# Optimization experiments

Hardware: AMD Instinct MI355X
Metric: run time of the kernel (lower is better)

## Reference

```python
import jax, jax.numpy as jnp
import numpy as np

EMB = 768
N_HEADS = 12
HEAD_DIM = EMB // N_HEADS


def setup_inputs() -> dict:
    key = jax.random.key(0)
    k_x, k_w1, k_b1, k_w2, k_b2 = jax.random.split(key, 5)
    B, T = 8, 1024
    s = 0.02
    return {
        "x": jax.random.normal(k_x, (B, T, EMB), dtype=jnp.float32),
        "w_attn": jax.random.normal(k_w1, (EMB, 3 * EMB), dtype=jnp.float32) * s,
        "b_attn": jax.random.normal(k_b1, (3 * EMB,), dtype=jnp.float32) * s,
        "w_proj": jax.random.normal(k_w2, (EMB, EMB), dtype=jnp.float32) * s,
        "b_proj": jax.random.normal(k_b2, (EMB,), dtype=jnp.float32) * s,
    }


def reference(x, w_attn, b_attn, w_proj, b_proj):
    B, T, C = x.shape
    qkv = x @ w_attn + b_attn                       # [B,T,3C]
    q, k, v = jnp.split(qkv, 3, axis=2)
    # [B,T,C] -> [B,H,T,D]
    q = q.reshape(B, T, N_HEADS, HEAD_DIM).transpose(0, 2, 1, 3)
    k = k.reshape(B, T, N_HEADS, HEAD_DIM).transpose(0, 2, 1, 3)
    v = v.reshape(B, T, N_HEADS, HEAD_DIM).transpose(0, 2, 1, 3)
    scale = HEAD_DIM ** -0.5
    att = jnp.einsum("bhqd,bhkd->bhqk", q, k) * scale  # [B,H,T,T]
    causal = jnp.tril(jnp.ones((T, T), dtype=bool))
    att = jnp.where(causal, att, -jnp.inf)
    att = jax.nn.softmax(att, axis=-1)
    out = jnp.einsum("bhqk,bhkd->bhqd", att, v)        # [B,H,T,D]
    out = out.transpose(0, 2, 1, 3).reshape(B, T, C)
    return out @ w_proj + b_proj
```

## Files before the change

### kernel.cpp

```cpp
#include <hip/hip_runtime.h>
#include <hip/hip_bf16.h>
#include <math.h>

#define BATCH 8
#define SEQ   1024
#define EMB   768
#define NH    12
#define HD    64
#define QKVW  (3 * EMB)
#define VOFF  (2 * EMB)

typedef short short8   __attribute__((ext_vector_type(8)));
typedef float floatx4  __attribute__((ext_vector_type(4)));

__device__ __forceinline__ short f2bf(float f) {
    union { float f; unsigned u; } v; v.f = f;
    unsigned r = (v.u + 0x7fffu + ((v.u >> 16) & 1u)) >> 16;
    return (short)r;
}

__device__ __forceinline__ void async_load16(const void* g, void* l) {
    __builtin_amdgcn_global_load_lds(
        (const __attribute__((address_space(1))) unsigned int*)g,
        (__attribute__((address_space(3))) unsigned int*)l, 16, 0, 0);
}

__global__ __launch_bounds__(256) void cvt_bf16(
    const float* __restrict__ in, short* __restrict__ out, int n8)
{
    const int i = blockIdx.x * 256 + threadIdx.x;
    if (i >= n8) return;
    const float4 a = ((const float4*)in)[2 * i];
    const float4 b = ((const float4*)in)[2 * i + 1];
    short8 s;
    s[0] = f2bf(a.x); s[1] = f2bf(a.y); s[2] = f2bf(a.z); s[3] = f2bf(a.w);
    s[4] = f2bf(b.x); s[5] = f2bf(b.y); s[6] = f2bf(b.z); s[7] = f2bf(b.w);
    ((short8*)out)[i] = s;
}

__global__ __launch_bounds__(256) void transpose_to_bf16(
    const float* __restrict__ in, short* __restrict__ outT, int R, int C)
{
    __shared__ float t[32][33];
    const int c0 = blockIdx.x * 32, r0 = blockIdx.y * 32;
    const int lx = threadIdx.x & 31, ly = threadIdx.x >> 5;
    #pragma unroll
    for (int i = 0; i < 32; i += 8)
        t[ly + i][lx] = in[(size_t)(r0 + ly + i) * C + c0 + lx];
    __syncthreads();
    #pragma unroll
    for (int i = 0; i < 32; i += 8)
        outT[(size_t)(c0 + ly + i) * R + r0 + lx] = f2bf(t[lx][ly + i]);
}

#define GBK 64

template <int MODE>
__global__ __launch_bounds__(256) void gemm_bf16(
    const short* __restrict__ A, const short* __restrict__ Bt,
    const float* __restrict__ bias, void* __restrict__ Cout,
    short* __restrict__ vt, int M, int N, int K)
{
    __shared__ __align__(16) short As[128 * GBK];
    __shared__ __align__(16) short Bs[128 * GBK];

    const int tid  = threadIdx.x;
    const int wave = tid >> 6;
    const int lane = tid & 63;
    const int ln15 = lane & 15;
    const int quad = lane >> 4;
    const int wr   = (wave >> 1) * 64;
    const int wc   = (wave & 1) * 64;
    const int row0 = blockIdx.y * 128;
    const int col0 = blockIdx.x * 128;

    const bool trans = (MODE == 0) || (col0 < VOFF);

    floatx4 acc[4][4];
    #pragma unroll
    for (int i = 0; i < 4; ++i)
        #pragma unroll
        for (int j = 0; j < 4; ++j) acc[i][j] = (floatx4){0.f, 0.f, 0.f, 0.f};

    for (int k0 = 0; k0 < K; k0 += GBK) {
        __syncthreads();
        #pragma unroll
        for (int p = 0; p < 4; ++p) {
            const int id  = p * 256 + tid;
            const int row = id >> 3;
            const int c   = (id & 7) ^ (row & 7);
            async_load16(A  + (size_t)(row0 + row) * K + k0 + c * 8, &As[id * 8]);
            async_load16(Bt + (size_t)(col0 + row) * K + k0 + c * 8, &Bs[id * 8]);
        }
        __syncthreads();

        #pragma unroll
        for (int half = 0; half < 2; ++half) {
            short8 af[4], bf[4];
            #pragma unroll
            for (int t = 0; t < 4; ++t) {
                const int ch = ((quad + half * 4) ^ (ln15 & 7)) * 8;
                af[t] = *(const short8*)&As[(wr + t * 16 + ln15) * GBK + ch];
                bf[t] = *(const short8*)&Bs[(wc + t * 16 + ln15) * GBK + ch];
            }
            if (trans) {
                #pragma unroll
                for (int i = 0; i < 4; ++i)
                    #pragma unroll
                    for (int j = 0; j < 4; ++j)
                        acc[i][j] = __builtin_amdgcn_mfma_f32_16x16x32_bf16(bf[j], af[i], acc[i][j], 0, 0, 0);
            } else {
                #pragma unroll
                for (int i = 0; i < 4; ++i)
                    #pragma unroll
                    for (int j = 0; j < 4; ++j)
                        acc[i][j] = __builtin_amdgcn_mfma_f32_16x16x32_bf16(af[i], bf[j], acc[i][j], 0, 0, 0);
            }
        }
    }

    if (MODE == 1 && !trans) {
        #pragma unroll
        for (int j = 0; j < 4; ++j) {
            const int c  = col0 + wc + j * 16 + ln15;
            const float bv = bias[c];
            const int c2 = c - VOFF;
            #pragma unroll
            for (int i = 0; i < 4; ++i) {
                const int r = row0 + wr + i * 16 + quad * 4;
                union { short s[4]; unsigned long long u; } pk;
                #pragma unroll
                for (int reg = 0; reg < 4; ++reg)
                    pk.s[reg] = f2bf(acc[i][j][reg] + bv);
                *(unsigned long long*)&vt[(size_t)(r >> 10) * (EMB * SEQ) +
                                          (size_t)c2 * SEQ + (r & 1023)] = pk.u;
            }
        }
    } else {
        float4 b4[4];
        #pragma unroll
        for (int j = 0; j < 4; ++j)
            b4[j] = *(const float4*)&bias[col0 + wc + j * 16 + quad * 4];
        #pragma unroll
        for (int i = 0; i < 4; ++i) {
            const int r = row0 + wr + i * 16 + ln15;
            #pragma unroll
            for (int j = 0; j < 4; ++j) {
                const int c = col0 + wc + j * 16 + quad * 4;
                if (MODE == 1) {
                    union { short s[4]; unsigned long long u; } pk;
                    pk.s[0] = f2bf(acc[i][j][0] + b4[j].x);
                    pk.s[1] = f2bf(acc[i][j][1] + b4[j].y);
                    pk.s[2] = f2bf(acc[i][j][2] + b4[j].z);
                    pk.s[3] = f2bf(acc[i][j][3] + b4[j].w);
                    *(unsigned long long*)&((short*)Cout)[(size_t)r * N + c] = pk.u;
                } else {
                    float4 v;
                    v.x = acc[i][j][0] + b4[j].x;
                    v.y = acc[i][j][1] + b4[j].y;
                    v.z = acc[i][j][2] + b4[j].z;
                    v.w = acc[i][j][3] + b4[j].w;
                    *(float4*)&((float*)Cout)[(size_t)r * N + c] = v;
                }
            }
        }
    }
}

#define LDK 72

__global__ __launch_bounds__(256) void attn_mfma(
    const short* __restrict__ qkv, const short* __restrict__ vt,
    short* __restrict__ out)
{
    __shared__ __align__(16) short Ks[64 * LDK];
    __shared__ __align__(16) short Vt[64 * LDK];
    __shared__ __align__(16) short Ps[4 * 16 * LDK];

    const int tid  = threadIdx.x;
    const int wave = tid >> 6;
    const int lane = tid & 63;
    const int ln15 = lane & 15;
    const int quad = lane >> 4;

    const int qc = 15 - (int)(blockIdx.x / (BATCH * NH));
    const int bh = blockIdx.x % (BATCH * NH);
    const int h  = bh % NH;
    const int b  = bh / NH;

    const int q0w = qc * 64 + wave * 16;

    const short* qkv_b = qkv + (size_t)b * SEQ * QKVW + h * HD;
    const short* Kg  = qkv_b + EMB;
    const short* Vtg = vt + ((size_t)b * EMB + h * HD) * SEQ;

    short8 qf[2];
    {
        const short* qrow = qkv_b + (size_t)(q0w + ln15) * QKVW;
        qf[0] = *(const short8*)(qrow + quad * 8);
        qf[1] = *(const short8*)(qrow + quad * 8 + 32);
    }

    floatx4 o[4];
    #pragma unroll
    for (int i = 0; i < 4; ++i) o[i] = (floatx4){0.f, 0.f, 0.f, 0.f};
    float lp[4] = {0.f, 0.f, 0.f, 0.f};

    const int rr = tid >> 3;
    const int c8 = (tid & 7) * 8;

    for (int kt = 0; kt <= qc; ++kt) {
        #pragma unroll
        for (int p = 0; p < 2; ++p) {
            const int r2 = rr + p * 32;
            *(uint4*)&Ks[r2 * LDK + c8] =
                *(const uint4*)(Kg + (size_t)(kt * 64 + r2) * QKVW + c8);
            *(uint4*)&Vt[r2 * LDK + c8] =
                *(const uint4*)(Vtg + (size_t)r2 * SEQ + kt * 64 + c8);
        }
        __syncthreads();

        floatx4 s[4];
        #pragma unroll
        for (int i = 0; i < 4; ++i) s[i] = (floatx4){0.f, 0.f, 0.f, 0.f};
        #pragma unroll
        for (int st = 0; st < 2; ++st)
            #pragma unroll
            for (int sub = 0; sub < 4; ++sub) {
                const short8 kf = *(const short8*)&Ks[(ln15 + sub * 16) * LDK + quad * 8 + st * 32];
                s[sub] = __builtin_amdgcn_mfma_f32_16x16x32_bf16(qf[st], kf, s[sub], 0, 0, 0);
            }

        const bool diag = (kt == qc);
        #pragma unroll
        for (int sub = 0; sub < 4; ++sub)
            #pragma unroll
            for (int reg = 0; reg < 4; ++reg) {
                float pv = __expf(s[sub][reg] * 0.125f);
                if (diag && (ln15 + sub * 16 > wave * 16 + quad * 4 + reg)) pv = 0.f;
                s[sub][reg] = pv;
            }
        #pragma unroll
        for (int reg = 0; reg < 4; ++reg)
            lp[reg] += (s[0][reg] + s[1][reg]) + (s[2][reg] + s[3][reg]);

        short* Pw = &Ps[wave * 16 * LDK];
        #pragma unroll
        for (int sub = 0; sub < 4; ++sub)
            #pragma unroll
            for (int reg = 0; reg < 4; ++reg) {
                const int qr   = quad * 4 + reg;
                const int kr8  = sub * 2 + (ln15 >> 3);
                const int slot = (kr8 + 5 * quad + reg) & 7;
                Pw[qr * LDK + slot * 8 + (ln15 & 7)] = f2bf(s[sub][reg]);
            }

        short8 pf[2];
        #pragma unroll
        for (int st = 0; st < 2; ++st) {
            const int slot = ((quad + 4 * st) + 5 * (ln15 >> 2) + (ln15 & 3)) & 7;
            pf[st] = *(const short8*)&Pw[ln15 * LDK + slot * 8];
        }

        #pragma unroll
        for (int st = 0; st < 2; ++st)
            #pragma unroll
            for (int sub = 0; sub < 4; ++sub) {
                const short8 vf = *(const short8*)&Vt[(ln15 + sub * 16) * LDK + quad * 8 + st * 32];
                o[sub] = __builtin_amdgcn_mfma_f32_16x16x32_bf16(pf[st], vf, o[sub], 0, 0, 0);
            }

        __syncthreads();
    }

    #pragma unroll
    for (int reg = 0; reg < 4; ++reg) {
        float t = lp[reg];
        #pragma unroll
        for (int off = 1; off <= 8; off <<= 1)
            t += __shfl_xor(t, off, 64);
        const float inv = 1.0f / t;
        const size_t row = (size_t)(b * SEQ + q0w + quad * 4 + reg) * EMB + h * HD;
        #pragma unroll
        for (int sub = 0; sub < 4; ++sub)
            out[row + ln15 + sub * 16] = f2bf(o[sub][reg] * inv);
    }
}

extern "C" void kernel_launch(void* const* d_in, const int* in_sizes, int n_in,
                              void* d_out, int out_size, void* d_ws, size_t ws_size,
                              hipStream_t stream)
{
    const float* x      = (const float*)d_in[0];
    const float* w_attn = (const float*)d_in[1];
    const float* b_attn = (const float*)d_in[2];
    const float* w_proj = (const float*)d_in[3];
    const float* b_proj = (const float*)d_in[4];
    float* out = (float*)d_out;

    const int M = BATCH * SEQ;

    short* xb    = (short*)d_ws;
    short* waT   = xb    + (size_t)M * EMB;
    short* wpT   = waT   + (size_t)QKVW * EMB;
    short* qkvb  = wpT   + (size_t)EMB * EMB;
    short* vtb   = qkvb  + (size_t)M * QKVW;
    short* attnb = vtb   + (size_t)BATCH * EMB * SEQ;

    dim3 blk(256);

    cvt_bf16<<<dim3((M * EMB) / 8 / 256), blk, 0, stream>>>(x, xb, (M * EMB) / 8);
    transpose_to_bf16<<<dim3(QKVW / 32, EMB / 32), blk, 0, stream>>>(w_attn, waT, EMB, QKVW);
    transpose_to_bf16<<<dim3(EMB / 32, EMB / 32), blk, 0, stream>>>(w_proj, wpT, EMB, EMB);

    gemm_bf16<1><<<dim3(QKVW / 128, M / 128), blk, 0, stream>>>(
        xb, waT, b_attn, qkvb, vtb, M, QKVW, EMB);

    attn_mfma<<<dim3(16 * BATCH * NH), blk, 0, stream>>>(qkvb, vtb, attnb);

    gemm_bf16<0><<<dim3(EMB / 128, M / 128), blk, 0, stream>>>(
        attnb, wpT, b_proj, out, nullptr, M, EMB, EMB);
}
```

Measured before the change: 218.0 us.

## Add 256x256-tile, 8-wave pipelined QKV GEMM with staged async loads

Replaces the 128x128 QKV projection GEMM with a dedicated 256x256 tile kernel that runs 8 waves per block. It double-buffers global-to-LDS async loads in quarter-tile stages interleaved with MFMA phases, using explicit waitcnt, barriers and priority hints. It also adds XOR-swizzled LDS addressing and an XCD-aware block remap. The aim is more reuse per tile and better overlap of loads with compute, at the cost of 128KB LDS per block, fewer blocks (288) and tricky hand-placed synchronisation.

```diff
diff --git a/kernel.cpp b/kernel.cpp
--- a/kernel.cpp
+++ b/kernel.cpp
@@ -167,6 +167,180 @@
     }
 }
 
+#define NT12 (EMB / 64)
+
+#define BAR()    do { asm volatile("" ::: "memory"); __builtin_amdgcn_s_barrier(); \
+                      asm volatile("" ::: "memory"); } while (0)
+#define LGKM0()  asm volatile("s_waitcnt lgkmcnt(0)" ::: "memory")
+#define VMC0()   asm volatile("s_waitcnt vmcnt(0)" ::: "memory")
+#define VMC2()   asm volatile("s_waitcnt vmcnt(2)" ::: "memory")
+#define VMC8()   asm volatile("s_waitcnt vmcnt(8)" ::: "memory")
+#define SCHED0() __builtin_amdgcn_sched_barrier(0)
+#define PRIO1()  __builtin_amdgcn_s_setprio(1)
+#define PRIO0()  __builtin_amdgcn_s_setprio(0)
+
+#define LDA(bf_, r_, q_) (*(const short8*)&As[bf_][(r_) * 64 + ((((q_)) ^ ((r_) & 7)) << 3)])
+#define LDB(bf_, r_, q_) (*(const short8*)&Bs[bf_][(r_) * 64 + ((((q_)) ^ ((r_) & 7)) << 3)])
+
+#define MMA8(IB, JB)                                                                   \
+    _Pragma("unroll")                                                                  \
+    for (int mi = 0; mi < 4; ++mi)                                                     \
+        _Pragma("unroll")                                                              \
+        for (int nj = 0; nj < 2; ++nj)                                                 \
+            _Pragma("unroll")                                                          \
+            for (int kk = 0; kk < 2; ++kk) {                                           \
+                if (vpath)                                                             \
+                    acc[(IB) + mi][(JB) + nj] = __builtin_amdgcn_mfma_f32_16x16x32_bf16( \
+                        a[mi][kk], b[(JB) + nj][kk], acc[(IB) + mi][(JB) + nj], 0, 0, 0); \
+                else                                                                   \
+                    acc[(IB) + mi][(JB) + nj] = __builtin_amdgcn_mfma_f32_16x16x32_bf16( \
+                        b[(JB) + nj][kk], a[mi][kk], acc[(IB) + mi][(JB) + nj], 0, 0, 0); \
+            }
+
+__global__ __launch_bounds__(512, 2) void gemm_qkv_256(
+    const short* __restrict__ A, const short* __restrict__ Bt,
+    const float* __restrict__ bias, short* __restrict__ qkvb,
+    short* __restrict__ vt)
+{
+    __shared__ __align__(16) short As[2][256 * 64];
+    __shared__ __align__(16) short Bs[2][256 * 64];
+
+    const int tid  = threadIdx.x;
+    const int wave = tid >> 6;
+    const int lane = tid & 63;
+    const int ln15 = lane & 15;
+    const int quad = lane >> 4;
+    const int wm   = wave >> 2;
+    const int wn   = wave & 3;
+
+    const int orig = blockIdx.x;
+    const int wg   = (orig & 7) * 36 + (orig >> 3);
+    const int bx   = wg % (QKVW / 256);
+    const int by   = wg / (QKVW / 256);
+    const int row0 = by * 256;
+    const int col0 = bx * 256;
+    const bool vpath = (col0 >= VOFF);
+
+    const short* Ag = A  + (size_t)row0 * EMB;
+    const short* Bg = Bt + (size_t)col0 * EMB;
+
+    auto stage_half = [&](int t, int h) {
+        if (t >= NT12) return;
+        const int buf   = t & 1;
+        const int k0    = t * 64;
+        const int rbase = (h & 1) * 128;
+        short* lb       = (h < 2) ? &As[buf][rbase * 64] : &Bs[buf][rbase * 64];
+        const short* gb = (h < 2) ? Ag : Bg;
+        #pragma unroll
+        for (int p = 0; p < 2; ++p) {
+            const int id  = p * 512 + tid;
+            const int row = rbase + (id >> 3);
+            const int c   = (id & 7) ^ (row & 7);
+            async_load16(gb + (size_t)row * EMB + k0 + c * 8, lb + (size_t)id * 8);
+        }
+    };
+
+    floatx4 acc[8][4];
+    #pragma unroll
+    for (int i = 0; i < 8; ++i)
+        #pragma unroll
+        for (int j = 0; j < 4; ++j) acc[i][j] = (floatx4){0.f, 0.f, 0.f, 0.f};
+
+    short8 a[4][2];
+    short8 b[4][2];
+
+    #pragma unroll
+    for (int h = 0; h < 4; ++h) stage_half(0, h);
+    #pragma unroll
+    for (int h = 0; h < 4; ++h) stage_half(1, h);
+    VMC8();
+    BAR();
+
+    const int ar0 = wm * 128 + ln15;
+    const int br0 = wn * 64 + ln15;
+
+    for (int kt = 0; kt < NT12; ++kt) {
+        const int buf = kt & 1;
+
+        #pragma unroll
+        for (int mi = 0; mi < 4; ++mi)
+            #pragma unroll
+            for (int kk = 0; kk < 2; ++kk)
+                a[mi][kk] = LDA(buf, ar0 + mi * 16, quad + kk * 4);
+        #pragma unroll
+        for (int nj = 0; nj < 2; ++nj)
+            #pragma unroll
+            for (int kk = 0; kk < 2; ++kk)
+                b[nj][kk] = LDB(buf, br0 + nj * 16, quad + kk * 4);
+        if (kt > 0) stage_half(kt + 1, 1);
+        BAR(); LGKM0(); SCHED0();
+        PRIO1(); MMA8(0, 0); PRIO0();
+        BAR();
+
+        #pragma unroll
+        for (int nj = 2; nj < 4; ++nj)
+            #pragma unroll
+            for (int kk = 0; kk < 2; ++kk)
+                b[nj][kk] = LDB(buf, br0 + nj * 16, quad + kk * 4);
+        if (kt > 0) stage_half(kt + 1, 2);
+        BAR(); LGKM0(); SCHED0();
+        PRIO1(); MMA8(0, 2); PRIO0();
+        BAR();
+
+        #pragma unroll
+        for (int mi = 0; mi < 4; ++mi)
+            #pragma unroll
+            for (int kk = 0; kk < 2; ++kk)
+                a[mi][kk] = LDA(buf, ar0 + 64 + mi * 16, quad + kk * 4);
+        if (kt > 0) stage_half(kt + 1, 3);
+        BAR(); LGKM0(); SCHED0();
+        PRIO1(); MMA8(4, 2); PRIO0();
+        BAR();
+
+        stage_half(kt + 2, 0);
+        BAR(); SCHED0();
+        PRIO1(); MMA8(4, 0); PRIO0();
+        if (kt + 2 < NT12) { VMC2(); }
+        else              { VMC0(); }
+        BAR();
+    }
+
+    if (!vpath) {
+        #pragma unroll
+        for (int j = 0; j < 4; ++j) {
+            const float4 b4 = *(const float4*)&bias[col0 + wn * 64 + j * 16 + quad * 4];
+            #pragma unroll
+            for (int i = 0; i < 8; ++i) {
+                const int r = row0 + wm * 128 + i * 16 + ln15;
+                const int c = col0 + wn * 64 + j * 16 + quad * 4;
+                union { short s[4]; unsigned long long u; } pk;
+                pk.s[0] = f2bf(acc[i][j][0] + b4.x);
+                pk.s[1] = f2bf(acc[i][j][1] + b4.y);
+                pk.s[2] = f2bf(acc[i][j][2] + b4.z);
+                pk.s[3] = f2bf(acc[i][j][3] + b4.w);
+                *(unsigned long long*)&qkvb[(size_t)r * QKVW + c] = pk.u;
+            }
+        }
+    } else {
+        #pragma unroll
+        for (int j = 0; j < 4; ++j) {
+            const int c  = col0 + wn * 64 + j * 16 + ln15;
+            const float bv = bias[c];
+            const int c2 = c - VOFF;
+            #pragma unroll
+            for (int i = 0; i < 8; ++i) {
+                const int r = row0 + wm * 128 + i * 16 + quad * 4;
+                union { short s[4]; unsigned long long u; } pk;
+                #pragma unroll
+                for (int reg = 0; reg < 4; ++reg)
+                    pk.s[reg] = f2bf(acc[i][j][reg] + bv);
+                *(unsigned long long*)&vt[(size_t)(r >> 10) * (EMB * SEQ) +
+                                          (size_t)c2 * SEQ + (r & 1023)] = pk.u;
+            }
+        }
+    }
+}
+
 #define LDK 72
 
 __global__ __launch_bounds__(256) void attn_mfma(
@@ -313,8 +487,8 @@
     transpose_to_bf16<<<dim3(QKVW / 32, EMB / 32), blk, 0, stream>>>(w_attn, waT, EMB, QKVW);
     transpose_to_bf16<<<dim3(EMB / 32, EMB / 32), blk, 0, stream>>>(w_proj, wpT, EMB, EMB);
 
-    gemm_bf16<1><<<dim3(QKVW / 128, M / 128), blk, 0, stream>>>(
-        xb, waT, b_attn, qkvb, vtb, M, QKVW, EMB);
+    gemm_qkv_256<<<dim3((QKVW / 256) * (M / 256)), dim3(512), 0, stream>>>(
+        xb, waT, b_attn, qkvb, vtb);
 
     attn_mfma<<<dim3(16 * BATCH * NH), blk, 0, stream>>>(qkvb, vtb, attnb);
 
```

Result: slower. 237.0 us (+8.7%).

## Replace GEMM with double-buffered 128x192 pipelined kernel using six waves

Applied to the files above, without the earlier changes.

The bf16 GEMM becomes a 384-thread kernel with 128x192 tiles and double-buffered LDS. Async global-to-LDS loads for the next K tiles are staged while MFMAs run, using explicit barriers, waitcnts and setprio. Blocks are remapped so neighbouring workgroups share tiles. The aim is to hide global-load latency behind compute and improve reuse, at the cost of more LDS, fragile hand-tuned synchronisation, and a tile shape that must divide the column boundaries at VOFF and N.

```diff
diff --git a/kernel.cpp b/kernel.cpp
--- a/kernel.cpp
+++ b/kernel.cpp
@@ -53,73 +53,148 @@
         outT[(size_t)(c0 + ly + i) * R + r0 + lx] = f2bf(t[lx][ly + i]);
 }
 
-#define GBK 64
+#define NT12 (EMB / 64)
+
+#define BAR()    do { asm volatile("" ::: "memory"); __builtin_amdgcn_s_barrier(); \
+                      asm volatile("" ::: "memory"); } while (0)
+#define LGKM0()  asm volatile("s_waitcnt lgkmcnt(0)" ::: "memory")
+#define VMC0()   asm volatile("s_waitcnt vmcnt(0)" ::: "memory")
+#define VMC4()   asm volatile("s_waitcnt vmcnt(4)" ::: "memory")
+#define SCHED0() __builtin_amdgcn_sched_barrier(0)
+#define PRIO1()  __builtin_amdgcn_s_setprio(1)
+#define PRIO0()  __builtin_amdgcn_s_setprio(0)
+
+#define LDA8(bf_, r_, q_) (*(const short8*)&As[bf_][(r_) * 64 + ((((q_)) ^ ((r_) & 7)) << 3)])
+#define LDB8(bf_, r_, q_) (*(const short8*)&Bs[bf_][(r_) * 64 + ((((q_)) ^ ((r_) & 7)) << 3)])
+
+#define MMA_T2(JB)                                                           \
+    _Pragma("unroll")                                                        \
+    for (int kk = 0; kk < 2; ++kk)                                           \
+        _Pragma("unroll")                                                    \
+        for (int mi = 0; mi < 4; ++mi)                                       \
+            _Pragma("unroll")                                                \
+            for (int nj = 0; nj < 2; ++nj)                                   \
+                acc[mi][(JB) + nj] =                                         \
+                    __builtin_amdgcn_mfma_f32_16x16x32_bf16(                 \
+                        b[(JB) + nj][kk], a[mi][kk],                         \
+                        acc[mi][(JB) + nj], 0, 0, 0);
+
+#define MMA_D2(JB)                                                           \
+    _Pragma("unroll")                                                        \
+    for (int kk = 0; kk < 2; ++kk)                                           \
+        _Pragma("unroll")                                                    \
+        for (int mi = 0; mi < 4; ++mi)                                       \
+            _Pragma("unroll")                                                \
+            for (int nj = 0; nj < 2; ++nj)                                   \
+                acc[mi][(JB) + nj] =                                         \
+                    __builtin_amdgcn_mfma_f32_16x16x32_bf16(                 \
+                        a[mi][kk], b[(JB) + nj][kk],                         \
+                        acc[mi][(JB) + nj], 0, 0, 0);
+
+#define KLOOP2(MM)                                                           \
+    for (int kt = 0; kt < NT12; ++kt) {                                      \
+        const int buf = kt & 1;                                              \
+                 \
+        _Pragma("unroll")                                                    \
+        for (int mi = 0; mi < 4; ++mi)                                       \
+            _Pragma("unroll")                                                \
+            for (int kk = 0; kk < 2; ++kk)                                   \
+                a[mi][kk] = LDA8(buf, ar0 + mi * 16, quad + kk * 4);         \
+        _Pragma("unroll")                                                    \
+        for (int nj = 0; nj < 2; ++nj)                                       \
+            _Pragma("unroll")                                                \
+            for (int kk = 0; kk < 2; ++kk)                                   \
+                b[nj][kk] = LDB8(buf, br0 + nj * 16, quad + kk * 4);         \
+        if (kt + 1 < NT12) stage_B(kt + 1);                                  \
+        BAR(); LGKM0(); SCHED0();                                            \
+        PRIO1(); MM(0); PRIO0();                                             \
+        BAR();                                                               \
+                     \
+        _Pragma("unroll")                                                    \
+        for (int nj = 2; nj < 4; ++nj)                                       \
+            _Pragma("unroll")                                                \
+            for (int kk = 0; kk < 2; ++kk)                                   \
+                b[nj][kk] = LDB8(buf, br0 + nj * 16, quad + kk * 4);         \
+        if (kt + 2 < NT12) stage_A(kt + 2);                                  \
+        BAR(); LGKM0(); SCHED0();                                            \
+        PRIO1(); MM(2); PRIO0();                                             \
+        if (kt + 2 < NT12) {                                                 \
+            if (wuni < 4) { VMC4(); } else { VMC0(); }                       \
+        } else if (kt + 1 < NT12) { VMC0(); }                                \
+        BAR();                                                               \
+    }
 
 template <int MODE>
-__global__ __launch_bounds__(256) void gemm_bf16(
+__global__ __launch_bounds__(384, 3) void gemm_pipe(
     const short* __restrict__ A, const short* __restrict__ Bt,
     const float* __restrict__ bias, void* __restrict__ Cout,
-    short* __restrict__ vt, int M, int N, int K)
-{
-    __shared__ __align__(16) short As[128 * GBK];
-    __shared__ __align__(16) short Bs[128 * GBK];
+    short* __restrict__ vt, int N, int nbx)
+{
+    __shared__ __align__(16) short As[2][128 * 64];
+    __shared__ __align__(16) short Bs[2][192 * 64];
 
     const int tid  = threadIdx.x;
     const int wave = tid >> 6;
     const int lane = tid & 63;
     const int ln15 = lane & 15;
     const int quad = lane >> 4;
-    const int wr   = (wave >> 1) * 64;
-    const int wc   = (wave & 1) * 64;
-    const int row0 = blockIdx.y * 128;
-    const int col0 = blockIdx.x * 128;
-
-    const bool trans = (MODE == 0) || (col0 < VOFF);
-
-    floatx4 acc[4][4];
-    #pragma unroll
-    for (int i = 0; i < 4; ++i)
-        #pragma unroll
-        for (int j = 0; j < 4; ++j) acc[i][j] = (floatx4){0.f, 0.f, 0.f, 0.f};
-
-    for (int k0 = 0; k0 < K; k0 += GBK) {
-        __syncthreads();
+    const int wm   = wave / 3;
+    const int wn   = wave % 3;
+    const int wuni = __builtin_amdgcn_readfirstlane(wave);
+
+    const int orig = blockIdx.x;
+    const int wg   = (orig & 7) * (8 * nbx) + (orig >> 3);
+    const int bx   = wg % nbx;
+    const int by   = wg / nbx;
+    const int row0 = by * 128;
+    const int col0 = bx * 192;
+    const bool vpath = (MODE == 1) && (col0 >= VOFF);
+
+    const short* Ag = A  + (size_t)row0 * EMB;
+    const short* Bg = Bt + (size_t)col0 * EMB;
+
+    auto stage_A = [&](int t) {
+        if (wave >= 4) return;
+        const int buf = t & 1;
         #pragma unroll
         for (int p = 0; p < 4; ++p) {
-            const int id  = p * 256 + tid;
+            const int id  = (wave * 4 + p) * 64 + lane;
             const int row = id >> 3;
             const int c   = (id & 7) ^ (row & 7);
-            async_load16(A  + (size_t)(row0 + row) * K + k0 + c * 8, &As[id * 8]);
-            async_load16(Bt + (size_t)(col0 + row) * K + k0 + c * 8, &Bs[id * 8]);
-        }
-        __syncthreads();
-
-        #pragma unroll
-        for (int half = 0; half < 2; ++half) {
-            short8 af[4], bf[4];
-            #pragma unroll
-            for (int t = 0; t < 4; ++t) {
-                const int ch = ((quad + half * 4) ^ (ln15 & 7)) * 8;
-                af[t] = *(const short8*)&As[(wr + t * 16 + ln15) * GBK + ch];
-                bf[t] = *(const short8*)&Bs[(wc + t * 16 + ln15) * GBK + ch];
-            }
-            if (trans) {
-                #pragma unroll
-                for (int i = 0; i < 4; ++i)
-                    #pragma unroll
-                    for (int j = 0; j < 4; ++j)
-                        acc[i][j] = __builtin_amdgcn_mfma_f32_16x16x32_bf16(bf[j], af[i], acc[i][j], 0, 0, 0);
-            } else {
-                #pragma unroll
-                for (int i = 0; i < 4; ++i)
-                    #pragma unroll
-                    for (int j = 0; j < 4; ++j)
-                        acc[i][j] = __builtin_amdgcn_mfma_f32_16x16x32_bf16(af[i], bf[j], acc[i][j], 0, 0, 0);
-            }
-        }
-    }
-
-    if (MODE == 1 && !trans) {
+            async_load16(Ag + (size_t)row * EMB + t * 64 + c * 8, &As[buf][id * 8]);
+        }
+    };
+    auto stage_B = [&](int t) {
+        const int buf = t & 1;
+        #pragma unroll
+        for (int p = 0; p < 4; ++p) {
+            const int id  = (wave * 4 + p) * 64 + lane;
+            const int row = id >> 3;
+            const int c   = (id & 7) ^ (row & 7);
+            async_load16(Bg + (size_t)row * EMB + t * 64 + c * 8, &Bs[buf][id * 8]);
+        }
+    };
+
+    floatx4 acc[4][4];
+    #pragma unroll
+    for (int i = 0; i < 4; ++i)
+        #pragma unroll
+        for (int j = 0; j < 4; ++j) acc[i][j] = (floatx4){0.f, 0.f, 0.f, 0.f};
+
+    short8 a[4][2];
+    short8 b[4][2];
+
+    stage_A(0); stage_B(0); stage_A(1);
+    if (wuni < 4) { VMC4(); } else { VMC0(); }
+    BAR();
+
+    const int ar0 = wm * 64 + ln15;
+    const int br0 = wn * 64 + ln15;
+
+    if (vpath) { KLOOP2(MMA_D2) } else { KLOOP2(MMA_T2) }
+
+    const int wr = wm * 64, wc = wn * 64;
+    if (vpath) {
         #pragma unroll
         for (int j = 0; j < 4; ++j) {
             const int c  = col0 + wc + j * 16 + ln15;
@@ -313,11 +388,11 @@
     transpose_to_bf16<<<dim3(QKVW / 32, EMB / 32), blk, 0, stream>>>(w_attn, waT, EMB, QKVW);
     transpose_to_bf16<<<dim3(EMB / 32, EMB / 32), blk, 0, stream>>>(w_proj, wpT, EMB, EMB);
 
-    gemm_bf16<1><<<dim3(QKVW / 128, M / 128), blk, 0, stream>>>(
-        xb, waT, b_attn, qkvb, vtb, M, QKVW, EMB);
+    gemm_pipe<1><<<dim3((M / 128) * (QKVW / 192)), dim3(384), 0, stream>>>(
+        xb, waT, b_attn, qkvb, vtb, QKVW, QKVW / 192);
 
     attn_mfma<<<dim3(16 * BATCH * NH), blk, 0, stream>>>(qkvb, vtb, attnb);
 
-    gemm_bf16<0><<<dim3(EMB / 128, M / 128), blk, 0, stream>>>(
-        attnb, wpT, b_proj, out, nullptr, M, EMB, EMB);
-}
+    gemm_pipe<0><<<dim3((M / 128) * (EMB / 192)), dim3(384), 0, stream>>>(
+        attnb, wpT, b_proj, out, nullptr, EMB, EMB / 192);
+}
```

New measurement: 206.6 us. -5.2%, faster.
